# Optimization experiments

Hardware: AMD Instinct MI355X
Metric: run time of the kernel (lower is better)

The kernel has to match this reference:

```python
import jax, jax.numpy as jnp
import numpy as np
from jax import lax

T = 2048          # tokens (batch*seq, module flattens to [-1, hidden])
H = 2048          # hidden_size
E = 32            # n_routed_experts
DF = 1024         # moe_intermediate_size
DS = 4096         # moe_shared_expert_intermediate_size
TOP_K = 6         # num_experts_per_tok
N_GROUP = 8
TOPK_GROUP = 4
SCALE = 2.5       # routed_scaling_factor
NORM_TOPK = True


def relu2(x):
    r = jax.nn.relu(x)
    return r * r


def setup_inputs() -> dict:
    key = jax.random.key(0)
    ks = jax.random.split(key, 7)
    s = 0.02
    return {
        "x": jax.random.normal(ks[0], (T, H), dtype=jnp.float32),
        "router_w": jax.random.normal(ks[1], (E, H), dtype=jnp.float32) * s,
        "router_b": jax.random.normal(ks[2], (E,), dtype=jnp.float32) * s,
        "w_up": jax.random.normal(ks[3], (E, H, DF), dtype=jnp.float32) * s,
        "w_down": jax.random.normal(ks[4], (E, DF, H), dtype=jnp.float32) * s,
        "shared_up": jax.random.normal(ks[5], (H, DS), dtype=jnp.float32) * s,
        "shared_down": jax.random.normal(ks[6], (DS, H), dtype=jnp.float32) * s,
    }


def _route(x, router_w, router_b):
    # router in fp32: logits -> sigmoid scores -> group-restricted top-k
    logits = x @ router_w.T                                  # [T, E]
    scores = jax.nn.sigmoid(logits)
    sfc = scores + router_b[None, :]                         # scores_for_choice
    gsize = E // N_GROUP
    grp = sfc.reshape(T, N_GROUP, gsize)
    group_scores = lax.top_k(grp, 2)[0].sum(-1)              # [T, n_group] sum of top-2
    _, gidx = lax.top_k(group_scores, TOPK_GROUP)            # [T, topk_group]
    group_mask = jax.nn.one_hot(gidx, N_GROUP, dtype=sfc.dtype).sum(1)  # [T, n_group]
    score_mask = jnp.repeat(group_mask, gsize, axis=1)       # [T, E]
    masked = jnp.where(score_mask > 0, sfc, 0.0)
    _, tidx = lax.top_k(masked, TOP_K)                       # [T, top_k]
    tw = jnp.take_along_axis(scores, tidx, axis=1)           # gather raw scores
    if NORM_TOPK:
        tw = tw / (tw.sum(-1, keepdims=True) + 1e-20)
    tw = tw * SCALE
    return tidx, tw


def reference(x, router_w, router_b, w_up, w_down, shared_up, shared_down):
    tidx, tw = _route(x, router_w, router_b)
    # dense combine weights [T, E]; equals sum of routed weights per expert
    combine = (jax.nn.one_hot(tidx, E, dtype=tw.dtype) * tw[..., None]).sum(1)
    # routed experts (no bias, so scaling before down_proj == scaling the output)
    h = jnp.einsum('td,edf->tef', x, w_up)                   # [T, E, DF]
    a = relu2(h) * combine[:, :, None]
    moe_out = jnp.einsum('tef,efd->td', a, w_down)           # [T, H]
    shared_out = relu2(x @ shared_up) @ shared_down
    return moe_out + shared_out
```

## Files before the change

### kernel.cpp

```cpp
#include <hip/hip_runtime.h>
#include <hip/hip_bf16.h>
#include <math.h>

#define T_TOK 2048
#define HID   2048
#define NE    32
#define DF    1024
#define DSZ   4096
#define TOPK  6
#define NGRP  8
#define TOPKG 4
#define RSCALE 2.5f
#define EXT_E 36
#define NSLOT 20480

typedef __attribute__((ext_vector_type(8))) short short8;
typedef __attribute__((ext_vector_type(4))) float f32x4;

typedef __attribute__((address_space(1))) const void gv1;
typedef __attribute__((address_space(3))) void lv3;

static __device__ __forceinline__ void gload16(const void* g, void* l) {
    __builtin_amdgcn_global_load_lds((gv1*)g, (lv3*)l, 16, 0, 0);
}

static __device__ __forceinline__ unsigned short f2b(float f) {
    union { float f; unsigned u; } v; v.f = f;
    unsigned r = v.u + 0x7fffu + ((v.u >> 16) & 1u);
    return (unsigned short)(r >> 16);
}

static __device__ void transpose_tile(const float* __restrict__ src, unsigned short* __restrict__ dst,
                                      int rs, int ds, int k0, int n0) {
    __shared__ unsigned short tile[64][72];
    int tid = threadIdx.x;
    int r = tid >> 4, c4 = (tid & 15) * 4;
    #pragma unroll
    for (int p = 0; p < 4; ++p) {
        int kk = r + p * 16;
        float4 v = *(const float4*)(src + (size_t)(k0 + kk) * rs + n0 + c4);
        tile[c4 + 0][kk] = f2b(v.x);
        tile[c4 + 1][kk] = f2b(v.y);
        tile[c4 + 2][kk] = f2b(v.z);
        tile[c4 + 3][kk] = f2b(v.w);
    }
    __syncthreads();
    int nr = tid >> 3, kc = (tid & 7) * 8;
    #pragma unroll
    for (int p = 0; p < 2; ++p) {
        int nn = nr + p * 32;
        short8 o;
        #pragma unroll
        for (int i = 0; i < 8; ++i) o[i] = tile[nn][kc + i];
        *(short8*)(dst + (size_t)(n0 + nn) * ds + k0 + kc) = o;
    }
}

static __device__ void router_body(int t, const float* __restrict__ x,
                                   const float* __restrict__ rw, const float* __restrict__ rb,
                                   int* __restrict__ tidx, float* __restrict__ tw,
                                   int* __restrict__ counts, unsigned short* __restrict__ xb) {
    __shared__ float xs[HID];
    __shared__ float part[256];
    __shared__ float scores[NE];
    __shared__ float sfc[NE];
    int tid = threadIdx.x;
    for (int i = tid; i < HID / 4; i += 256) {
        ((float4*)xs)[i] = ((const float4*)(x + (size_t)t * HID))[i];
    }
    __syncthreads();
    {
        float4 a = ((const float4*)xs)[tid * 2];
        float4 b = ((const float4*)xs)[tid * 2 + 1];
        short8 o;
        o[0] = (short)f2b(a.x); o[1] = (short)f2b(a.y); o[2] = (short)f2b(a.z); o[3] = (short)f2b(a.w);
        o[4] = (short)f2b(b.x); o[5] = (short)f2b(b.y); o[6] = (short)f2b(b.z); o[7] = (short)f2b(b.w);
        *(short8*)(xb + (size_t)t * HID + tid * 8) = o;
    }
    int e = tid & 31, ch = tid >> 5;
    const float* w = rw + (size_t)e * HID + ch * 256;
    const float* xv = xs + ch * 256;
    float p = 0.f;
    #pragma unroll 8
    for (int k = 0; k < 256; ++k) p += xv[k] * w[k];
    part[tid] = p;
    __syncthreads();
    if (tid < 32) {
        float l = 0.f;
        #pragma unroll
        for (int c = 0; c < 8; ++c) l += part[c * 32 + tid];
        float s = 1.f / (1.f + expf(-l));
        scores[tid] = s;
        sfc[tid] = s + rb[tid];
    }
    __syncthreads();
    if (tid == 0) {
        float gs[NGRP];
        for (int g = 0; g < NGRP; ++g) {
            float v[4];
            for (int i = 0; i < 4; ++i) v[i] = sfc[g * 4 + i];
            int bi = 0;
            for (int i = 1; i < 4; ++i) if (v[i] > v[bi]) bi = i;
            float m1 = v[bi]; v[bi] = -INFINITY;
            int bj = 0;
            for (int i = 1; i < 4; ++i) if (v[i] > v[bj]) bj = i;
            gs[g] = m1 + v[bj];
        }
        bool gsel[NGRP];
        for (int g = 0; g < NGRP; ++g) gsel[g] = false;
        for (int k = 0; k < TOPKG; ++k) {
            int bi = -1; float b = -INFINITY;
            for (int g = 0; g < NGRP; ++g)
                if (!gsel[g] && gs[g] > b) { b = gs[g]; bi = g; }
            gsel[bi] = true;
        }
        float masked[NE];
        for (int i = 0; i < NE; ++i) masked[i] = gsel[i >> 2] ? sfc[i] : 0.0f;
        int sel[TOPK]; float wv[TOPK]; float wsum = 0.f;
        for (int k = 0; k < TOPK; ++k) {
            int bi = -1; float b = -INFINITY;
            for (int i = 0; i < NE; ++i)
                if (masked[i] > b) { b = masked[i]; bi = i; }
            masked[bi] = -INFINITY;
            sel[k] = bi; wv[k] = scores[bi]; wsum += wv[k];
        }
        float inv = RSCALE / (wsum + 1e-20f);
        for (int k = 0; k < TOPK; ++k) {
            tidx[t * TOPK + k] = sel[k];
            tw[t * TOPK + k] = wv[k] * inv;
            atomicAdd(&counts[sel[k]], 1);
        }
    }
}

__global__ __launch_bounds__(256, 2)
void router_tup_kernel(const float* __restrict__ x, const float* __restrict__ rw,
                       const float* __restrict__ rb, const float* __restrict__ w_up,
                       const float* __restrict__ sh_up,
                       int* __restrict__ tidx, float* __restrict__ tw,
                       int* __restrict__ counts, unsigned short* __restrict__ xb,
                       unsigned short* __restrict__ bufU) {
    int bid = blockIdx.x;
    if (bid % 10 == 0) {
        router_body(bid / 10, x, rw, rb, tidx, tw, counts, xb);
    } else {
        int tile = bid - bid / 10 - 1;
        int tz = tile >> 9;
        int rem = tile & 511;
        int tn = rem & 15, tk = rem >> 4;
        const float* src; int rs;
        if (tz < NE) { src = w_up + (size_t)tz * HID * DF; rs = DF; }
        else         { src = sh_up + (size_t)(tz - NE) * DF; rs = DSZ; }
        transpose_tile(src, bufU + (size_t)tz * DF * HID, rs, HID, tk * 64, tn * 64);
    }
}

__global__ void scan_kernel(const int* __restrict__ counts, int* __restrict__ offsets) {
    if (threadIdx.x == 0) {
        int a = 0;
        for (int e2 = 0; e2 < NE; ++e2) { offsets[e2] = a; a += counts[e2]; }
        offsets[NE] = a;
        for (int j = 1; j <= 4; ++j) offsets[NE + j] = 12288 + j * T_TOK;
    }
}

__global__ void scatter_kernel(const int* __restrict__ tidx, const float* __restrict__ tw,
                               const int* __restrict__ offsets, int* __restrict__ cursors,
                               int* __restrict__ perm, float* __restrict__ pw,
                               int* __restrict__ slot_of) {
    int t = blockIdx.x * blockDim.x + threadIdx.x;
    if (t >= T_TOK) return;
    for (int k = 0; k < TOPK; ++k) {
        int e = tidx[t * TOPK + k];
        int pos = atomicAdd(&cursors[e], 1);
        int slot = offsets[e] + pos;
        perm[slot] = t;
        pw[slot] = tw[t * TOPK + k];
        slot_of[t * TOPK + k] = slot;
    }
    #pragma unroll
    for (int j = 0; j < 4; ++j) {
        int slot = 12288 + j * T_TOK + t;
        perm[slot] = t;
        pw[slot] = 1.0f;
    }
}

__global__ __launch_bounds__(256, 2)
void fused_up_kernel(const unsigned short* __restrict__ xb, const unsigned short* __restrict__ bufU,
                     const float* __restrict__ w_dn, const float* __restrict__ sh_dn,
                     unsigned short* __restrict__ bufD, unsigned short* __restrict__ act,
                     const int* __restrict__ offsets, const int* __restrict__ perm,
                     const float* __restrict__ pw) {
    int bid = blockIdx.x;
    if (bid % 5 != 0) {
        int tile = bid - bid / 5 - 1;
        int tz = tile >> 9;
        int rem = tile & 511;
        int tn = rem & 31, tk = rem >> 5;
        const float* src = (tz < NE) ? (w_dn + (size_t)tz * DF * HID)
                                     : (sh_dn + (size_t)(tz - NE) * DF * HID);
        transpose_tile(src, bufD + (size_t)tz * HID * DF, HID, DF, tk * 64, tn * 64);
        return;
    }
    int g = bid / 5;
    int bx = g & 7, by = (g >> 3) & 15, bz = g >> 7;
    constexpr int K = HID, N = DF;

    __shared__ __align__(16) char lds[32768];
    char* As = lds;
    char* Bs = lds + 16384;

    int tid = threadIdx.x;
    int lane = tid & 63, wvid = tid >> 6, wr = wvid >> 1, wc = wvid & 1;

    int off = offsets[bz], end = offsets[bz + 1];
    int row0 = off + by * 128;
    if (row0 >= end) return;
    int n0 = bx * 128;

    int lr = lane >> 3;
    int csrc = (((lane & 7) ^ lr) << 4);
    size_t abyte[4], bbyte[4];
    int ldsoff[4];
    const char* Bb = (const char*)bufU + (size_t)bz * ((size_t)N * K * 2);
    #pragma unroll
    for (int p = 0; p < 4; ++p) {
        int r = p * 32 + wvid * 8 + lr;
        int gr = row0 + r;
        if (gr > end - 1) gr = end - 1;
        abyte[p] = (size_t)perm[gr] * (K * 2);
        bbyte[p] = (size_t)(n0 + r) * (K * 2);
        ldsoff[p] = (p * 32 + wvid * 8) * 128;
    }

    f32x4 acc[4][4] = {};
    for (int k0 = 0; k0 < K; k0 += 64) {
        __syncthreads();
        #pragma unroll
        for (int p = 0; p < 4; ++p) {
            gload16((const char*)xb + abyte[p] + k0 * 2 + csrc, As + ldsoff[p]);
            gload16(Bb + bbyte[p] + k0 * 2 + csrc, Bs + ldsoff[p]);
        }
        __syncthreads();
        #pragma unroll
        for (int ks = 0; ks < 2; ++ks) {
            int kg = lane >> 4, r16 = lane & 15;
            short8 af[4], bfr[4];
            #pragma unroll
            for (int m = 0; m < 4; ++m) {
                int r = wr * 64 + m * 16 + r16;
                af[m] = *(const short8*)(As + r * 128 + ((ks * 64 + kg * 16) ^ ((r & 7) << 4)));
            }
            #pragma unroll
            for (int n = 0; n < 4; ++n) {
                int c = wc * 64 + n * 16 + r16;
                bfr[n] = *(const short8*)(Bs + c * 128 + ((ks * 64 + kg * 16) ^ ((c & 7) << 4)));
            }
            #pragma unroll
            for (int m = 0; m < 4; ++m)
                #pragma unroll
                for (int n = 0; n < 4; ++n)
                    acc[m][n] = __builtin_amdgcn_mfma_f32_16x16x32_bf16(af[m], bfr[n], acc[m][n], 0, 0, 0);
        }
    }

    int r16 = lane & 15, rg = lane >> 4;
    #pragma unroll
    for (int m = 0; m < 4; ++m) {
        #pragma unroll
        for (int j = 0; j < 4; ++j) {
            int rr = row0 + wr * 64 + m * 16 + rg * 4 + j;
            if (rr < end) {
                float scale = pw[rr];
                #pragma unroll
                for (int n = 0; n < 4; ++n) {
                    int cc = n0 + wc * 64 + n * 16 + r16;
                    float v = acc[m][n][j];
                    v = v > 0.f ? v * v : 0.f;
                    act[(size_t)rr * N + cc] = f2b(v * scale);
                }
            }
        }
    }
}

__global__ __launch_bounds__(256, 2)
void gemm_down_kernel(const unsigned short* __restrict__ act, const unsigned short* __restrict__ bufD,
                      float* __restrict__ slotout, const int* __restrict__ offsets) {
    constexpr int K = DF, N = HID;
    __shared__ __align__(16) char lds[32768];
    char* As = lds;
    char* Bs = lds + 16384;

    int tid = threadIdx.x;
    int lane = tid & 63, wvid = tid >> 6, wr = wvid >> 1, wc = wvid & 1;

    int bz = blockIdx.z;
    int off = offsets[bz], end = offsets[bz + 1];
    int row0 = off + blockIdx.y * 128;
    if (row0 >= end) return;
    int n0 = blockIdx.x * 128;

    int lr = lane >> 3;
    int csrc = (((lane & 7) ^ lr) << 4);
    size_t abyte[4], bbyte[4];
    int ldsoff[4];
    const char* Bb = (const char*)bufD + (size_t)bz * ((size_t)N * K * 2);
    #pragma unroll
    for (int p = 0; p < 4; ++p) {
        int r = p * 32 + wvid * 8 + lr;
        int gr = row0 + r;
        if (gr > end - 1) gr = end - 1;
        abyte[p] = (size_t)gr * (K * 2);
        bbyte[p] = (size_t)(n0 + r) * (K * 2);
        ldsoff[p] = (p * 32 + wvid * 8) * 128;
    }

    f32x4 acc[4][4] = {};
    for (int k0 = 0; k0 < K; k0 += 64) {
        __syncthreads();
        #pragma unroll
        for (int p = 0; p < 4; ++p) {
            gload16((const char*)act + abyte[p] + k0 * 2 + csrc, As + ldsoff[p]);
            gload16(Bb + bbyte[p] + k0 * 2 + csrc, Bs + ldsoff[p]);
        }
        __syncthreads();
        #pragma unroll
        for (int ks = 0; ks < 2; ++ks) {
            int kg = lane >> 4, r16 = lane & 15;
            short8 af[4], bfr[4];
            #pragma unroll
            for (int m = 0; m < 4; ++m) {
                int r = wr * 64 + m * 16 + r16;
                af[m] = *(const short8*)(As + r * 128 + ((ks * 64 + kg * 16) ^ ((r & 7) << 4)));
            }
            #pragma unroll
            for (int n = 0; n < 4; ++n) {
                int c = wc * 64 + n * 16 + r16;
                bfr[n] = *(const short8*)(Bs + c * 128 + ((ks * 64 + kg * 16) ^ ((c & 7) << 4)));
            }
            #pragma unroll
            for (int m = 0; m < 4; ++m)
                #pragma unroll
                for (int n = 0; n < 4; ++n)
                    acc[m][n] = __builtin_amdgcn_mfma_f32_16x16x32_bf16(af[m], bfr[n], acc[m][n], 0, 0, 0);
        }
    }

    int r16 = lane & 15, rg = lane >> 4;
    #pragma unroll
    for (int m = 0; m < 4; ++m) {
        #pragma unroll
        for (int j = 0; j < 4; ++j) {
            int rr = row0 + wr * 64 + m * 16 + rg * 4 + j;
            if (rr < end) {
                #pragma unroll
                for (int n = 0; n < 4; ++n) {
                    int cc = n0 + wc * 64 + n * 16 + r16;
                    slotout[(size_t)rr * N + cc] = acc[m][n][j];
                }
            }
        }
    }
}

__global__ void combine_kernel(const float* __restrict__ slotout, const int* __restrict__ slot_of,
                               float* __restrict__ out) {
    int t = blockIdx.x, tid = threadIdx.x;
    int s[10];
    #pragma unroll
    for (int k = 0; k < TOPK; ++k) s[k] = slot_of[t * TOPK + k];
    #pragma unroll
    for (int j = 0; j < 4; ++j) s[TOPK + j] = 12288 + j * T_TOK + t;
    #pragma unroll
    for (int p = 0; p < 2; ++p) {
        int c = (p * 256 + tid) * 4;
        float4 a = {0.f, 0.f, 0.f, 0.f};
        #pragma unroll
        for (int k = 0; k < 10; ++k) {
            float4 v = *(const float4*)(slotout + (size_t)s[k] * HID + c);
            a.x += v.x; a.y += v.y; a.z += v.z; a.w += v.w;
        }
        *(float4*)(out + (size_t)t * HID + c) = a;
    }
}

extern "C" void kernel_launch(void* const* d_in, const int* in_sizes, int n_in,
                              void* d_out, int out_size, void* d_ws, size_t ws_size,
                              hipStream_t stream) {
    const float* x     = (const float*)d_in[0];
    const float* rw    = (const float*)d_in[1];
    const float* rb    = (const float*)d_in[2];
    const float* w_up  = (const float*)d_in[3];
    const float* w_dn  = (const float*)d_in[4];
    const float* sh_up = (const float*)d_in[5];
    const float* sh_dn = (const float*)d_in[6];
    float* out = (float*)d_out;
    char* ws = (char*)d_ws;

    int*   counts  = (int*)(ws);
    int*   cursors = (int*)(ws + 128);
    int*   offsets = (int*)(ws + 256);
    int*   tidx    = (int*)(ws + 1024);
    float* tw      = (float*)(ws + 50176);
    int*   slot_of = (int*)(ws + 99328);
    int*   perm    = (int*)(ws + 148480);
    float* pw      = (float*)(ws + 230400);
    unsigned short* xb   = (unsigned short*)(ws + 312320);
    unsigned short* act  = (unsigned short*)(ws + 8700928);
    unsigned short* bufU = (unsigned short*)(ws + 50643968);
    unsigned short* bufD = (unsigned short*)(ws + 201638912);
    float* slotout       = (float*)(ws + 352633856);

    hipMemsetAsync(ws, 0, 256, stream);

    router_tup_kernel<<<20480, 256, 0, stream>>>(x, rw, rb, w_up, sh_up,
                                                 tidx, tw, counts, xb, bufU);
    scan_kernel<<<1, 64, 0, stream>>>(counts, offsets);
    scatter_kernel<<<(T_TOK + 255) / 256, 256, 0, stream>>>(tidx, tw, offsets, cursors,
                                                            perm, pw, slot_of);

    fused_up_kernel<<<23040, 256, 0, stream>>>(xb, bufU, w_dn, sh_dn, bufD, act,
                                               offsets, perm, pw);

    gemm_down_kernel<<<dim3(HID / 128, T_TOK / 128, EXT_E), 256, 0, stream>>>(
        act, bufD, slotout, offsets);

    combine_kernel<<<T_TOK, 256, 0, stream>>>(slotout, slot_of, out);
}
```

Measured before the change: 630.9 us.

## Split fused weight-transpose work into standalone kernels with wider tiles

Removes the fusion of weight transpose/bf16 conversion with the router and up-GEMM kernels and launches dedicated transpose kernels before each GEMM. The transpose tile becomes 128x32 with fp32 LDS staging and conversion on the output side, which gives wider vectorised reads and writes. The router and up-GEMM now run as plain kernels with their own grids. This gives up the overlap of transpose traffic with router and GEMM compute in exchange for simpler kernels, better occupancy and less branch divergence.

```diff
diff --git a/kernel.cpp b/kernel.cpp
--- a/kernel.cpp
+++ b/kernel.cpp
@@ -30,40 +30,16 @@
     return (unsigned short)(r >> 16);
 }
 
-static __device__ void transpose_tile(const float* __restrict__ src, unsigned short* __restrict__ dst,
-                                      int rs, int ds, int k0, int n0) {
-    __shared__ unsigned short tile[64][72];
-    int tid = threadIdx.x;
-    int r = tid >> 4, c4 = (tid & 15) * 4;
-    #pragma unroll
-    for (int p = 0; p < 4; ++p) {
-        int kk = r + p * 16;
-        float4 v = *(const float4*)(src + (size_t)(k0 + kk) * rs + n0 + c4);
-        tile[c4 + 0][kk] = f2b(v.x);
-        tile[c4 + 1][kk] = f2b(v.y);
-        tile[c4 + 2][kk] = f2b(v.z);
-        tile[c4 + 3][kk] = f2b(v.w);
-    }
-    __syncthreads();
-    int nr = tid >> 3, kc = (tid & 7) * 8;
-    #pragma unroll
-    for (int p = 0; p < 2; ++p) {
-        int nn = nr + p * 32;
-        short8 o;
-        #pragma unroll
-        for (int i = 0; i < 8; ++i) o[i] = tile[nn][kc + i];
-        *(short8*)(dst + (size_t)(n0 + nn) * ds + k0 + kc) = o;
-    }
-}
-
-static __device__ void router_body(int t, const float* __restrict__ x,
-                                   const float* __restrict__ rw, const float* __restrict__ rb,
-                                   int* __restrict__ tidx, float* __restrict__ tw,
-                                   int* __restrict__ counts, unsigned short* __restrict__ xb) {
+__global__ __launch_bounds__(256)
+void router_kernel(const float* __restrict__ x, const float* __restrict__ rw,
+                   const float* __restrict__ rb,
+                   int* __restrict__ tidx, float* __restrict__ tw,
+                   int* __restrict__ counts, unsigned short* __restrict__ xb) {
     __shared__ float xs[HID];
     __shared__ float part[256];
     __shared__ float scores[NE];
     __shared__ float sfc[NE];
+    int t = blockIdx.x;
     int tid = threadIdx.x;
     for (int i = tid; i < HID / 4; i += 256) {
         ((float4*)xs)[i] = ((const float4*)(x + (size_t)t * HID))[i];
@@ -130,28 +106,6 @@
             tw[t * TOPK + k] = wv[k] * inv;
             atomicAdd(&counts[sel[k]], 1);
         }
-    }
-}
-
-__global__ __launch_bounds__(256, 2)
-void router_tup_kernel(const float* __restrict__ x, const float* __restrict__ rw,
-                       const float* __restrict__ rb, const float* __restrict__ w_up,
-                       const float* __restrict__ sh_up,
-                       int* __restrict__ tidx, float* __restrict__ tw,
-                       int* __restrict__ counts, unsigned short* __restrict__ xb,
-                       unsigned short* __restrict__ bufU) {
-    int bid = blockIdx.x;
-    if (bid % 10 == 0) {
-        router_body(bid / 10, x, rw, rb, tidx, tw, counts, xb);
-    } else {
-        int tile = bid - bid / 10 - 1;
-        int tz = tile >> 9;
-        int rem = tile & 511;
-        int tn = rem & 15, tk = rem >> 4;
-        const float* src; int rs;
-        if (tz < NE) { src = w_up + (size_t)tz * HID * DF; rs = DF; }
-        else         { src = sh_up + (size_t)(tz - NE) * DF; rs = DSZ; }
-        transpose_tile(src, bufU + (size_t)tz * DF * HID, rs, HID, tk * 64, tn * 64);
     }
 }
 
@@ -186,27 +140,63 @@
     }
 }
 
+static __device__ __forceinline__ void transpose_tile_v2(
+        const float* __restrict__ src, unsigned short* __restrict__ dst,
+        int rs, int K, int k0, int n0) {
+    __shared__ float tile_t[32][132];
+    int t = threadIdx.x;
+    int kk0 = t >> 3;
+    int c4 = (t & 7) * 4;
+    #pragma unroll
+    for (int p = 0; p < 4; ++p) {
+        int kk = kk0 + 32 * p;
+        float4 v = *(const float4*)(src + (size_t)(k0 + kk) * rs + n0 + c4);
+        tile_t[c4 + 0][kk] = v.x;
+        tile_t[c4 + 1][kk] = v.y;
+        tile_t[c4 + 2][kk] = v.z;
+        tile_t[c4 + 3][kk] = v.w;
+    }
+    __syncthreads();
+    int n = t >> 3;
+    int kb = (t & 7) * 8;
+    #pragma unroll
+    for (int s = 0; s < 2; ++s) {
+        int kc = kb + 64 * s;
+        float4 a = *(const float4*)&tile_t[n][kc];
+        float4 b = *(const float4*)&tile_t[n][kc + 4];
+        short8 o;
+        o[0] = (short)f2b(a.x); o[1] = (short)f2b(a.y); o[2] = (short)f2b(a.z); o[3] = (short)f2b(a.w);
+        o[4] = (short)f2b(b.x); o[5] = (short)f2b(b.y); o[6] = (short)f2b(b.z); o[7] = (short)f2b(b.w);
+        *(short8*)(dst + (size_t)(n0 + n) * K + k0 + kc) = o;
+    }
+}
+
+__global__ __launch_bounds__(256)
+void transpose_up_kernel(const float* __restrict__ w_up, const float* __restrict__ sh_up,
+                         unsigned short* __restrict__ bufU) {
+    int z = blockIdx.z;
+    const float* src; int rs;
+    if (z < NE) { src = w_up + (size_t)z * HID * DF; rs = DF; }
+    else        { src = sh_up + (size_t)(z - NE) * DF; rs = DSZ; }
+    transpose_tile_v2(src, bufU + (size_t)z * DF * HID, rs, HID,
+                      blockIdx.y * 128, blockIdx.x * 32);
+}
+
+__global__ __launch_bounds__(256)
+void transpose_dn_kernel(const float* __restrict__ w_dn, const float* __restrict__ sh_dn,
+                         unsigned short* __restrict__ bufD) {
+    int z = blockIdx.z;
+    const float* src = (z < NE) ? (w_dn + (size_t)z * DF * HID)
+                                : (sh_dn + (size_t)(z - NE) * DF * HID);
+    transpose_tile_v2(src, bufD + (size_t)z * HID * DF, HID, DF,
+                      blockIdx.y * 128, blockIdx.x * 32);
+}
+
 __global__ __launch_bounds__(256, 2)
-void fused_up_kernel(const unsigned short* __restrict__ xb, const unsigned short* __restrict__ bufU,
-                     const float* __restrict__ w_dn, const float* __restrict__ sh_dn,
-                     unsigned short* __restrict__ bufD, unsigned short* __restrict__ act,
-                     const int* __restrict__ offsets, const int* __restrict__ perm,
-                     const float* __restrict__ pw) {
-    int bid = blockIdx.x;
-    if (bid % 5 != 0) {
-        int tile = bid - bid / 5 - 1;
-        int tz = tile >> 9;
-        int rem = tile & 511;
-        int tn = rem & 31, tk = rem >> 5;
-        const float* src = (tz < NE) ? (w_dn + (size_t)tz * DF * HID)
-                                     : (sh_dn + (size_t)(tz - NE) * DF * HID);
-        transpose_tile(src, bufD + (size_t)tz * HID * DF, HID, DF, tk * 64, tn * 64);
-        return;
-    }
-    int g = bid / 5;
-    int bx = g & 7, by = (g >> 3) & 15, bz = g >> 7;
+void gemm_up_kernel(const unsigned short* __restrict__ xb, const unsigned short* __restrict__ bufU,
+                    unsigned short* __restrict__ act, const int* __restrict__ offsets,
+                    const int* __restrict__ perm, const float* __restrict__ pw) {
     constexpr int K = HID, N = DF;
-
     __shared__ __align__(16) char lds[32768];
     char* As = lds;
     char* Bs = lds + 16384;
@@ -214,10 +204,11 @@
     int tid = threadIdx.x;
     int lane = tid & 63, wvid = tid >> 6, wr = wvid >> 1, wc = wvid & 1;
 
+    int bz = blockIdx.z;
     int off = offsets[bz], end = offsets[bz + 1];
-    int row0 = off + by * 128;
+    int row0 = off + blockIdx.y * 128;
     if (row0 >= end) return;
-    int n0 = bx * 128;
+    int n0 = blockIdx.x * 128;
 
     int lr = lane >> 3;
     int csrc = (((lane & 7) ^ lr) << 4);
@@ -415,15 +406,16 @@
 
     hipMemsetAsync(ws, 0, 256, stream);
 
-    router_tup_kernel<<<20480, 256, 0, stream>>>(x, rw, rb, w_up, sh_up,
-                                                 tidx, tw, counts, xb, bufU);
+    router_kernel<<<T_TOK, 256, 0, stream>>>(x, rw, rb, tidx, tw, counts, xb);
     scan_kernel<<<1, 64, 0, stream>>>(counts, offsets);
     scatter_kernel<<<(T_TOK + 255) / 256, 256, 0, stream>>>(tidx, tw, offsets, cursors,
                                                             perm, pw, slot_of);
 
-    fused_up_kernel<<<23040, 256, 0, stream>>>(xb, bufU, w_dn, sh_dn, bufD, act,
-                                               offsets, perm, pw);
-
+    transpose_up_kernel<<<dim3(32, 16, EXT_E), 256, 0, stream>>>(w_up, sh_up, bufU);
+    gemm_up_kernel<<<dim3(DF / 128, T_TOK / 128, EXT_E), 256, 0, stream>>>(
+        xb, bufU, act, offsets, perm, pw);
+
+    transpose_dn_kernel<<<dim3(64, 8, EXT_E), 256, 0, stream>>>(w_dn, sh_dn, bufD);
     gemm_down_kernel<<<dim3(HID / 128, T_TOK / 128, EXT_E), 256, 0, stream>>>(
         act, bufD, slotout, offsets);
 
```

New measurement: 600.5 us. -4.8%, faster.
